# Performance work log

Measured on AMD Instinct MI355X. Metric: run time of the kernel, lower is better.

Reference implementation:

```python
import jax, jax.numpy as jnp
import numpy as np

N, E, D, L = 50000, 800000, 128, 2
NEG_SLOPE = 0.2
LN_EPS = 1e-5


def setup_inputs() -> dict:
    key = jax.random.key(0)
    ks = jax.random.split(key, 6)
    scale = 1.0 / np.sqrt(D)
    x = jax.random.normal(ks[0], (N, D), dtype=jnp.float32)
    edge_index = jax.random.randint(ks[1], (2, E), 0, N, dtype=jnp.int64)
    W = jax.random.normal(ks[2], (L, D, D), dtype=jnp.float32) * scale
    att_src = jax.random.normal(ks[3], (L, D), dtype=jnp.float32) * scale
    att_dst = jax.random.normal(ks[4], (L, D), dtype=jnp.float32) * scale
    bias = jnp.zeros((L, D), dtype=jnp.float32)
    gamma = jnp.ones((L, D), dtype=jnp.float32)
    beta = jnp.zeros((L, D), dtype=jnp.float32)
    return {"x": x, "edge_index": edge_index, "W": W, "att_src": att_src,
            "att_dst": att_dst, "bias": bias, "gamma": gamma, "beta": beta}


def reference(x, edge_index, W, att_src, att_dst, bias, gamma, beta):
    # PyG GATConv (heads=1, concat=True, add_self_loops=True), eval mode
    # (attention/feature dropout disabled), followed by residual + LayerNorm.
    n = x.shape[0]
    loops = jnp.arange(n, dtype=edge_index.dtype)
    ei = jnp.concatenate([edge_index, jnp.stack([loops, loops])], axis=1)
    src, dst = ei[0], ei[1]  # messages flow src -> dst
    for l in range(W.shape[0]):
        h = x @ W[l]                              # [N, D]
        a_src = h @ att_src[l]                    # [N]
        a_dst = h @ att_dst[l]                    # [N]
        logit = jax.nn.leaky_relu(a_src[src] + a_dst[dst], NEG_SLOPE)  # [E+N]
        # segment softmax over incoming edges of each dst node
        m = jax.ops.segment_max(logit, dst, num_segments=n)
        e = jnp.exp(logit - m[dst])
        s = jax.ops.segment_sum(e, dst, num_segments=n)
        alpha = e / s[dst]
        msg = h[src] * alpha[:, None]             # [E+N, D]
        x_att = jax.ops.segment_sum(msg, dst, num_segments=n) + bias[l]
        # residual + LayerNorm
        y = x + x_att
        mu = jnp.mean(y, axis=-1, keepdims=True)
        var = jnp.var(y, axis=-1, keepdims=True)
        x = (y - mu) * jax.lax.rsqrt(var + LN_EPS) * gamma[l] + beta[l]
    return x
```

## Files before the change

kernel.cpp:

```cpp
#include <hip/hip_runtime.h>
#include <hip/hip_fp16.h>

#define D 128
#define NSLOPE 0.2f
#define LN_EPS 1e-5f
#define CAP 6144

typedef unsigned int uint;
typedef float f32x4 __attribute__((ext_vector_type(4)));
typedef _Float16 f16x8 __attribute__((ext_vector_type(8)));

__device__ __forceinline__ float leaky(float x) { return x > 0.f ? x : NSLOPE * x; }
__device__ __forceinline__ uint pkh(float a, float b) {
    __half2 h = __floats2half2_rn(a, b);
    return *reinterpret_cast<uint*>(&h);
}
__device__ __forceinline__ float2 h2f(uint u) {
    __half2 h = *reinterpret_cast<__half2*>(&u);
    return __half22float2(h);
}
__device__ __forceinline__ __half2 u2h2(uint u) {
    return *reinterpret_cast<__half2*>(&u);
}

__global__ __launch_bounds__(256) void k_bucket(const int* __restrict__ ei,
        int* __restrict__ gcur, uint* __restrict__ staging, int e, int nbuck) {
    __shared__ uint pr[4096];
    __shared__ int hist[256], gbase[256], c2[256];
    int t = threadIdx.x;
    int base = blockIdx.x * 4096;
    hist[t] = 0;
    c2[t] = 0;
    int nv = min(4096, e - base);
    for (int j = t; j < nv; j += 256) {
        int i = base + j;
        pr[j] = ((uint)ei[e + i] << 16) | (uint)ei[i];
    }
    __syncthreads();
    for (int j = t; j < nv; j += 256)
        atomicAdd(&hist[pr[j] >> 24], 1);
    __syncthreads();
    if (t < nbuck && hist[t] > 0)
        gbase[t] = t * CAP + atomicAdd(&gcur[t], hist[t]);
    __syncthreads();
    for (int j = t; j < nv; j += 256) {
        uint p = pr[j];
        int b = p >> 24;
        int pos = atomicAdd(&c2[b], 1);
        staging[gbase[b] + pos] = p;
    }
}

__global__ __launch_bounds__(256) void k_bfill2(const uint* __restrict__ staging,
        const int* __restrict__ gcur, int* __restrict__ rowptr,
        int* __restrict__ csr, int n, int nb) {
    __shared__ int sb[256];
    __shared__ int h[256];
    __shared__ int lds[256];
    __shared__ int c2[256];
    int b = blockIdx.x, t = threadIdx.x;
    sb[t] = (t < nb) ? gcur[t] : 0;
    h[t] = 0;
    c2[t] = 0;
    __syncthreads();
    for (int off = 1; off < 256; off <<= 1) {
        int u = (t >= off) ? sb[t - off] : 0;
        __syncthreads();
        sb[t] += u;
        __syncthreads();
    }
    int ebase = (b == 0) ? 0 : sb[b - 1];
    int cnt = gcur[b];
    for (int i = t; i < cnt; i += 256)
        atomicAdd(&h[(staging[b * CAP + i] >> 16) & 255], 1);
    __syncthreads();
    int d = h[t];
    lds[t] = d;
    __syncthreads();
    for (int off = 1; off < 256; off <<= 1) {
        int u = (t >= off) ? lds[t - off] : 0;
        __syncthreads();
        lds[t] += u;
        __syncthreads();
    }
    int rp = ebase + lds[t] - d;
    int node = b * 256 + t;
    if (node < n) rowptr[node] = rp;
    if (b == 0 && t == 0) rowptr[n] = sb[nb - 1];
    __syncthreads();
    h[t] = rp;
    __syncthreads();
    for (int i = t; i < cnt; i += 256) {
        uint p = staging[b * CAP + i];
        int dn = (p >> 16) & 255;
        int r = atomicAdd(&c2[dn], 1);
        csr[h[dn] + r] = (int)(p & 0xffffu);
    }
}

__global__ __launch_bounds__(256) void k_wt(const float* __restrict__ W,
                                            uint* __restrict__ wth) {
    __shared__ float T[128][17];
    int t = threadIdx.x;
    int layer = blockIdx.x >> 3;
    int c0 = (blockIdx.x & 7) * 16;
    const float* Wl = W + (size_t)layer * D * D;
    uint* wl = wth + (size_t)layer * D * 64;
    #pragma unroll
    for (int pass = 0; pass < 2; ++pass) {
        int k = pass * 64 + (t >> 2);
        int c = (t & 3) * 4;
        float4 v = *(const float4*)&Wl[k * D + c0 + c];
        T[k][c] = v.x; T[k][c + 1] = v.y; T[k][c + 2] = v.z; T[k][c + 3] = v.w;
    }
    __syncthreads();
    int cw = t >> 4;
    int k0 = (t & 15) * 8;
    uint4 uh;
    uh.x = pkh(T[k0 + 0][cw], T[k0 + 1][cw]);
    uh.y = pkh(T[k0 + 2][cw], T[k0 + 3][cw]);
    uh.z = pkh(T[k0 + 4][cw], T[k0 + 5][cw]);
    uh.w = pkh(T[k0 + 6][cw], T[k0 + 7][cw]);
    *(uint4*)&wl[(c0 + cw) * 64 + (t & 15) * 4] = uh;
}

template <bool F16IN>
__global__ __launch_bounds__(256) void k_gemm2(const float* __restrict__ xf,
        const uint* __restrict__ xh, const uint* __restrict__ wth,
        const float* __restrict__ avs, const float* __restrict__ avd,
        uint* __restrict__ hb, float* __restrict__ asrc, float* __restrict__ adst, int n) {
    __shared__ char XH[64 * 256];
    __shared__ char WH[128 * 256];
    __shared__ float psL[256], pdL[256];

    int t = threadIdx.x;
    int brow = blockIdx.x * 64;
    int rows = min(64, n - brow);

    #pragma unroll
    for (int i = 0; i < 8; ++i) {
        int f = t + 256 * i;
        int row = f >> 5, k4 = f & 31;
        uint2 ph = make_uint2(0u, 0u);
        if (row < rows) {
            if (F16IN) {
                ph = *(const uint2*)&xh[(size_t)(brow + row) * 64 + k4 * 2];
            } else {
                float4 v = *(const float4*)&xf[(size_t)(brow + row) * D + k4 * 4];
                ph = make_uint2(pkh(v.x, v.y), pkh(v.z, v.w));
            }
        }
        int off = row * 256 + k4 * 8;
        int swz = (row & 7) << 4;
        *(uint2*)(XH + (off ^ swz)) = ph;
    }
    #pragma unroll
    for (int i = 0; i < 8; ++i) {
        int f = t + 256 * i;
        int col = f >> 4, j = f & 15;
        uint4 vh = *(const uint4*)&wth[col * 64 + j * 4];
        int off = col * 256 + j * 16;
        int swz = (col & 7) << 4;
        *(uint4*)(WH + (off ^ swz)) = vh;
    }
    __syncthreads();

    int wave = t >> 6, lane = t & 63;
    int l15 = lane & 15, lk = lane >> 4;

    f32x4 acc[4][2];
    #pragma unroll
    for (int rt = 0; rt < 4; ++rt)
        #pragma unroll
        for (int ct = 0; ct < 2; ++ct)
            acc[rt][ct] = (f32x4){0.f, 0.f, 0.f, 0.f};

    #pragma unroll
    for (int ks = 0; ks < 4; ++ks) {
        f16x8 a[4], b[2];
        #pragma unroll
        for (int rt = 0; rt < 4; ++rt) {
            int row = rt * 16 + l15;
            int off = row * 256 + (ks * 32 + lk * 8) * 2;
            int swz = (row & 7) << 4;
            a[rt] = *(const f16x8*)(XH + (off ^ swz));
        }
        #pragma unroll
        for (int ct = 0; ct < 2; ++ct) {
            int col = wave * 32 + ct * 16 + l15;
            int off = col * 256 + (ks * 32 + lk * 8) * 2;
            int swz = (col & 7) << 4;
            b[ct] = *(const f16x8*)(WH + (off ^ swz));
        }
        #pragma unroll
        for (int rt = 0; rt < 4; ++rt)
            #pragma unroll
            for (int ct = 0; ct < 2; ++ct)
                acc[rt][ct] = __builtin_amdgcn_mfma_f32_16x16x32_f16(a[rt], b[ct], acc[rt][ct], 0, 0, 0);
    }

    float avs_lo = avs[wave * 32 + l15], avs_hi = avs[wave * 32 + 16 + l15];
    float avd_lo = avd[wave * 32 + l15], avd_hi = avd[wave * 32 + 16 + l15];
    #pragma unroll
    for (int rt = 0; rt < 4; ++rt) {
        #pragma unroll
        for (int j = 0; j < 4; ++j) {
            float ps = acc[rt][0][j] * avs_lo + acc[rt][1][j] * avs_hi;
            float pd = acc[rt][0][j] * avd_lo + acc[rt][1][j] * avd_hi;
            #pragma unroll
            for (int off = 8; off; off >>= 1) {
                ps += __shfl_xor(ps, off);
                pd += __shfl_xor(pd, off);
            }
            int row = rt * 16 + lk * 4 + j;
            if (l15 == 0) { psL[wave * 64 + row] = ps; pdL[wave * 64 + row] = pd; }
        }
    }
    #pragma unroll
    for (int rt = 0; rt < 4; ++rt) {
        #pragma unroll
        for (int j = 0; j < 4; ++j) {
            int row = rt * 16 + lk * 4 + j;
            if (row < rows)
                hb[(size_t)(brow + row) * 64 + wave * 16 + l15] =
                    pkh(acc[rt][0][j], acc[rt][1][j]);
        }
    }
    __syncthreads();
    if (t < 64 && t < rows) {
        asrc[brow + t] = psL[t] + psL[64 + t] + psL[128 + t] + psL[192 + t];
        adst[brow + t] = pdL[t] + pdL[64 + t] + pdL[128 + t] + pdL[192 + t];
    }
}

template <int MODE>
__global__ __launch_bounds__(256) void k_attn(const float* __restrict__ xf,
        const uint* __restrict__ xh, const uint* __restrict__ hb,
        const float* __restrict__ asrc, const float* __restrict__ adst,
        const int* __restrict__ rowptr, const int* __restrict__ csr,
        const float* __restrict__ bias, const float* __restrict__ gamma,
        const float* __restrict__ beta, float* __restrict__ out,
        uint* __restrict__ outh, int n) {
    int node = blockIdx.x * 16 + (threadIdx.x >> 4);
    if (node >= n) return;
    int sl = threadIdx.x & 15;
    int base_lo = (sl >> 2) * 32 + (sl & 3) * 4;

    float a_i = adst[node];
    float slg = leaky(asrc[node] + a_i);
    int rs = rowptr[node], re = rowptr[node + 1];

    float m_g = slg, ssum = 1.f;
    __half2 acch[4];
    {
        uint4 q = *(const uint4*)&hb[(size_t)node * 64 + sl * 4];
        acch[0] = u2h2(q.x); acch[1] = u2h2(q.y);
        acch[2] = u2h2(q.z); acch[3] = u2h2(q.w);
    }

    for (int e = rs; e < re; e += 2) {
        int c1 = min(e + 1, re - 1);
        int s0 = csr[e], s1 = csr[c1];
        uint4 q0 = *(const uint4*)&hb[(size_t)s0 * 64 + sl * 4];
        uint4 q1 = *(const uint4*)&hb[(size_t)s1 * 64 + sl * 4];
        float lg0 = leaky(asrc[s0] + a_i);
        float lg1 = (e + 1 < re) ? leaky(asrc[s1] + a_i) : -1e30f;
        float nm = fmaxf(m_g, fmaxf(lg0, lg1));
        if (nm > m_g) {
            float sc = __expf(m_g - nm);
            ssum *= sc;
            __half2 sch = __half2half2(__float2half(sc));
            #pragma unroll
            for (int j = 0; j < 4; ++j) acch[j] = __hmul2(acch[j], sch);
            m_g = nm;
        }
        float w0 = __expf(lg0 - nm);
        float w1 = (e + 1 < re) ? __expf(lg1 - nm) : 0.f;
        ssum += w0 + w1;
        __half2 w0h = __half2half2(__float2half(w0));
        __half2 w1h = __half2half2(__float2half(w1));
        acch[0] = __hfma2(w0h, u2h2(q0.x), acch[0]);
        acch[1] = __hfma2(w0h, u2h2(q0.y), acch[1]);
        acch[2] = __hfma2(w0h, u2h2(q0.z), acch[2]);
        acch[3] = __hfma2(w0h, u2h2(q0.w), acch[3]);
        acch[0] = __hfma2(w1h, u2h2(q1.x), acch[0]);
        acch[1] = __hfma2(w1h, u2h2(q1.y), acch[1]);
        acch[2] = __hfma2(w1h, u2h2(q1.z), acch[2]);
        acch[3] = __hfma2(w1h, u2h2(q1.w), acch[3]);
    }

    float inv = 1.f / ssum;
    float acc[8];
    {
        float2 f0 = __half22float2(acch[0]);
        float2 f1 = __half22float2(acch[1]);
        float2 f2 = __half22float2(acch[2]);
        float2 f3 = __half22float2(acch[3]);
        acc[0] = f0.x * inv; acc[1] = f1.x * inv; acc[2] = f2.x * inv; acc[3] = f3.x * inv;
        acc[4] = f0.y * inv; acc[5] = f1.y * inv; acc[6] = f2.y * inv; acc[7] = f3.y * inv;
    }

    float x0, x1, x2, x3, x4, x5, x6, x7;
    if (MODE == 0) {
        float4 xa = *(const float4*)&xf[(size_t)node * D + base_lo];
        float4 xb = *(const float4*)&xf[(size_t)node * D + base_lo + 16];
        x0 = xa.x; x1 = xa.y; x2 = xa.z; x3 = xa.w;
        x4 = xb.x; x5 = xb.y; x6 = xb.z; x7 = xb.w;
    } else {
        uint2 ua = *(const uint2*)&xh[(size_t)node * 64 + (base_lo >> 1)];
        uint2 ub = *(const uint2*)&xh[(size_t)node * 64 + (base_lo >> 1) + 8];
        float2 fa0 = h2f(ua.x), fa1 = h2f(ua.y), fb0 = h2f(ub.x), fb1 = h2f(ub.y);
        x0 = fa0.x; x1 = fa0.y; x2 = fa1.x; x3 = fa1.y;
        x4 = fb0.x; x5 = fb0.y; x6 = fb1.x; x7 = fb1.y;
    }
    float4 ba = *(const float4*)&bias[base_lo];
    float4 bb = *(const float4*)&bias[base_lo + 16];
    float y[8];
    y[0] = x0 + acc[0] + ba.x;
    y[1] = x1 + acc[1] + ba.y;
    y[2] = x2 + acc[2] + ba.z;
    y[3] = x3 + acc[3] + ba.w;
    y[4] = x4 + acc[4] + bb.x;
    y[5] = x5 + acc[5] + bb.y;
    y[6] = x6 + acc[6] + bb.z;
    y[7] = x7 + acc[7] + bb.w;

    float s1 = 0.f, s2 = 0.f;
    #pragma unroll
    for (int j = 0; j < 8; ++j) { s1 += y[j]; s2 += y[j] * y[j]; }
    #pragma unroll
    for (int off = 1; off <= 8; off <<= 1) {
        s1 += __shfl_xor(s1, off);
        s2 += __shfl_xor(s2, off);
    }
    float mu = s1 * (1.f / D);
    float var = s2 * (1.f / D) - mu * mu;
    float rstd = rsqrtf(var + LN_EPS);

    float4 ga = *(const float4*)&gamma[base_lo];
    float4 gb = *(const float4*)&gamma[base_lo + 16];
    float4 bta = *(const float4*)&beta[base_lo];
    float4 btb = *(const float4*)&beta[base_lo + 16];
    float o0 = (y[0] - mu) * rstd * ga.x + bta.x;
    float o1 = (y[1] - mu) * rstd * ga.y + bta.y;
    float o2 = (y[2] - mu) * rstd * ga.z + bta.z;
    float o3 = (y[3] - mu) * rstd * ga.w + bta.w;
    float o4 = (y[4] - mu) * rstd * gb.x + btb.x;
    float o5 = (y[5] - mu) * rstd * gb.y + btb.y;
    float o6 = (y[6] - mu) * rstd * gb.z + btb.z;
    float o7 = (y[7] - mu) * rstd * gb.w + btb.w;
    if (MODE == 0) {
        uint2 oa = make_uint2(pkh(o0, o1), pkh(o2, o3));
        uint2 ob = make_uint2(pkh(o4, o5), pkh(o6, o7));
        *(uint2*)&outh[(size_t)node * 64 + (base_lo >> 1)] = oa;
        *(uint2*)&outh[(size_t)node * 64 + (base_lo >> 1) + 8] = ob;
    } else {
        *(float4*)&out[(size_t)node * D + base_lo] = make_float4(o0, o1, o2, o3);
        *(float4*)&out[(size_t)node * D + base_lo + 16] = make_float4(o4, o5, o6, o7);
    }
}

extern "C" void kernel_launch(void* const* d_in, const int* in_sizes, int n_in,
                              void* d_out, int out_size, void* d_ws, size_t ws_size,
                              hipStream_t stream) {
    const float* x       = (const float*)d_in[0];
    const int*   ei      = (const int*)d_in[1];
    const float* W       = (const float*)d_in[2];
    const float* att_src = (const float*)d_in[3];
    const float* att_dst = (const float*)d_in[4];
    const float* bias    = (const float*)d_in[5];
    const float* gamma   = (const float*)d_in[6];
    const float* beta    = (const float*)d_in[7];
    float* out = (float*)d_out;

    const int N = in_sizes[0] / D;
    const int E = in_sizes[1] / 2;
    const int NBUCK = (N + 255) / 256;

    char* base = (char*)d_ws;
    size_t off = 0;
    auto alloc = [&](size_t bytes) {
        char* p = base + off;
        off += (bytes + 255) & ~(size_t)255;
        return p;
    };
    uint*  hb      = (uint*)alloc((size_t)N * 64 * 4);
    uint*  xh16    = (uint*)alloc((size_t)N * 64 * 4);
    float* asrc    = (float*)alloc((size_t)N * 4);
    float* adst    = (float*)alloc((size_t)N * 4);
    int*   rowptr  = (int*)alloc((size_t)(N + 1) * 4);
    int*   csr     = (int*)alloc((size_t)E * 4);
    uint*  staging = (uint*)alloc((size_t)NBUCK * CAP * 4);
    int*   gcur    = (int*)alloc((size_t)NBUCK * 4);
    uint*  wth     = (uint*)alloc((size_t)2 * D * 64 * 4);

    hipMemsetAsync(gcur, 0, (size_t)NBUCK * 4, stream);
    k_bucket<<<(E + 4095) / 4096, 256, 0, stream>>>(ei, gcur, staging, E, NBUCK);
    k_bfill2<<<NBUCK, 256, 0, stream>>>(staging, gcur, rowptr, csr, N, NBUCK);
    k_wt<<<16, 256, 0, stream>>>(W, wth);

    const int nblk_node = (N + 15) / 16;
    const int nblk_gemm = (N + 63) / 64;

    k_gemm2<false><<<nblk_gemm, 256, 0, stream>>>(x, nullptr, wth, att_src, att_dst,
                                                  hb, asrc, adst, N);
    k_attn<0><<<nblk_node, 256, 0, stream>>>(x, nullptr, hb, asrc, adst, rowptr, csr,
                                             bias, gamma, beta, nullptr, xh16, N);
    k_gemm2<true><<<nblk_gemm, 256, 0, stream>>>(nullptr, xh16, wth + (size_t)D * 64,
                                                 att_src + D, att_dst + D,
                                                 hb, asrc, adst, N);
    k_attn<1><<<nblk_node, 256, 0, stream>>>(nullptr, xh16, hb, asrc, adst, rowptr, csr,
                                             bias + D, gamma + D, beta + D, out, nullptr, N);
}
```

Before: 145.8 us.

## Fuse edge bucketing into first GEMM launch and merge weight prep with counter reset

Folds the memset of the bucket counters into the weight-transpose kernel, and runs the edge-bucketing blocks in the same grid as the layer-0 GEMM blocks, selected by block index. This cuts launch count and lets the two independent stages overlap on the GPU instead of running one after the other. The fused kernel reserves the larger GEMM shared-memory footprint for every block, which may lower occupancy for the bucketing blocks.

New measurement: 137.9 us. 1.06x faster.

```diff
diff --git a/kernel.cpp b/kernel.cpp
--- a/kernel.cpp
+++ b/kernel.cpp
@@ -23,12 +23,45 @@
     return *reinterpret_cast<__half2*>(&u);
 }
 
-__global__ __launch_bounds__(256) void k_bucket(const int* __restrict__ ei,
-        int* __restrict__ gcur, uint* __restrict__ staging, int e, int nbuck) {
-    __shared__ uint pr[4096];
-    __shared__ int hist[256], gbase[256], c2[256];
+__global__ __launch_bounds__(256) void k_prep(const float* __restrict__ W,
+        uint* __restrict__ wth, int* __restrict__ gcur, int nbuck) {
+    __shared__ float T[128][17];
     int t = threadIdx.x;
-    int base = blockIdx.x * 4096;
+    if (blockIdx.x == 16) {
+        if (t < nbuck) gcur[t] = 0;
+        return;
+    }
+    int layer = blockIdx.x >> 3;
+    int c0 = (blockIdx.x & 7) * 16;
+    const float* Wl = W + (size_t)layer * D * D;
+    uint* wl = wth + (size_t)layer * D * 64;
+    #pragma unroll
+    for (int pass = 0; pass < 2; ++pass) {
+        int k = pass * 64 + (t >> 2);
+        int c = (t & 3) * 4;
+        float4 v = *(const float4*)&Wl[k * D + c0 + c];
+        T[k][c] = v.x; T[k][c + 1] = v.y; T[k][c + 2] = v.z; T[k][c + 3] = v.w;
+    }
+    __syncthreads();
+    int cw = t >> 4;
+    int k0 = (t & 15) * 8;
+    uint4 uh;
+    uh.x = pkh(T[k0 + 0][cw], T[k0 + 1][cw]);
+    uh.y = pkh(T[k0 + 2][cw], T[k0 + 3][cw]);
+    uh.z = pkh(T[k0 + 4][cw], T[k0 + 5][cw]);
+    uh.w = pkh(T[k0 + 6][cw], T[k0 + 7][cw]);
+    *(uint4*)&wl[(c0 + cw) * 64 + (t & 15) * 4] = uh;
+}
+
+__device__ __forceinline__ void bucket_body(char* SMEM, int bid,
+        const int* __restrict__ ei, int* __restrict__ gcur,
+        uint* __restrict__ staging, int e, int nbuck) {
+    uint* pr   = (uint*)SMEM;
+    int* hist  = (int*)(SMEM + 16384);
+    int* gbase = (int*)(SMEM + 17408);
+    int* c2    = (int*)(SMEM + 18432);
+    int t = threadIdx.x;
+    int base = bid * 4096;
     hist[t] = 0;
     c2[t] = 0;
     int nv = min(4096, e - base);
@@ -49,6 +82,138 @@
         int pos = atomicAdd(&c2[b], 1);
         staging[gbase[b] + pos] = p;
     }
+}
+
+template <bool F16IN>
+__device__ __forceinline__ void gemm_body(char* SMEM, int bid,
+        const float* __restrict__ xf, const uint* __restrict__ xh,
+        const uint* __restrict__ wth, const float* __restrict__ avs,
+        const float* __restrict__ avd, uint* __restrict__ hb,
+        float* __restrict__ asrc, float* __restrict__ adst, int n) {
+    char* XH   = SMEM;
+    char* WH   = SMEM + 16384;
+    float* psL = (float*)(SMEM + 49152);
+    float* pdL = (float*)(SMEM + 50176);
+
+    int t = threadIdx.x;
+    int brow = bid * 64;
+    int rows = min(64, n - brow);
+
+    #pragma unroll
+    for (int i = 0; i < 8; ++i) {
+        int f = t + 256 * i;
+        int row = f >> 5, k4 = f & 31;
+        uint2 ph = make_uint2(0u, 0u);
+        if (row < rows) {
+            if (F16IN) {
+                ph = *(const uint2*)&xh[(size_t)(brow + row) * 64 + k4 * 2];
+            } else {
+                float4 v = *(const float4*)&xf[(size_t)(brow + row) * D + k4 * 4];
+                ph = make_uint2(pkh(v.x, v.y), pkh(v.z, v.w));
+            }
+        }
+        int off = row * 256 + k4 * 8;
+        int swz = (row & 7) << 4;
+        *(uint2*)(XH + (off ^ swz)) = ph;
+    }
+    #pragma unroll
+    for (int i = 0; i < 8; ++i) {
+        int f = t + 256 * i;
+        int col = f >> 4, j = f & 15;
+        uint4 vh = *(const uint4*)&wth[col * 64 + j * 4];
+        int off = col * 256 + j * 16;
+        int swz = (col & 7) << 4;
+        *(uint4*)(WH + (off ^ swz)) = vh;
+    }
+    __syncthreads();
+
+    int wave = t >> 6, lane = t & 63;
+    int l15 = lane & 15, lk = lane >> 4;
+
+    f32x4 acc[4][2];
+    #pragma unroll
+    for (int rt = 0; rt < 4; ++rt)
+        #pragma unroll
+        for (int ct = 0; ct < 2; ++ct)
+            acc[rt][ct] = (f32x4){0.f, 0.f, 0.f, 0.f};
+
+    #pragma unroll
+    for (int ks = 0; ks < 4; ++ks) {
+        f16x8 a[4], b[2];
+        #pragma unroll
+        for (int rt = 0; rt < 4; ++rt) {
+            int row = rt * 16 + l15;
+            int off = row * 256 + (ks * 32 + lk * 8) * 2;
+            int swz = (row & 7) << 4;
+            a[rt] = *(const f16x8*)(XH + (off ^ swz));
+        }
+        #pragma unroll
+        for (int ct = 0; ct < 2; ++ct) {
+            int col = wave * 32 + ct * 16 + l15;
+            int off = col * 256 + (ks * 32 + lk * 8) * 2;
+            int swz = (col & 7) << 4;
+            b[ct] = *(const f16x8*)(WH + (off ^ swz));
+        }
+        #pragma unroll
+        for (int rt = 0; rt < 4; ++rt)
+            #pragma unroll
+            for (int ct = 0; ct < 2; ++ct)
+                acc[rt][ct] = __builtin_amdgcn_mfma_f32_16x16x32_f16(a[rt], b[ct], acc[rt][ct], 0, 0, 0);
+    }
+
+    float avs_lo = avs[wave * 32 + l15], avs_hi = avs[wave * 32 + 16 + l15];
+    float avd_lo = avd[wave * 32 + l15], avd_hi = avd[wave * 32 + 16 + l15];
+    #pragma unroll
+    for (int rt = 0; rt < 4; ++rt) {
+        #pragma unroll
+        for (int j = 0; j < 4; ++j) {
+            float ps = acc[rt][0][j] * avs_lo + acc[rt][1][j] * avs_hi;
+            float pd = acc[rt][0][j] * avd_lo + acc[rt][1][j] * avd_hi;
+            #pragma unroll
+            for (int off = 8; off; off >>= 1) {
+                ps += __shfl_xor(ps, off);
+                pd += __shfl_xor(pd, off);
+            }
+            int row = rt * 16 + lk * 4 + j;
+            if (l15 == 0) { psL[wave * 64 + row] = ps; pdL[wave * 64 + row] = pd; }
+        }
+    }
+    #pragma unroll
+    for (int rt = 0; rt < 4; ++rt) {
+        #pragma unroll
+        for (int j = 0; j < 4; ++j) {
+            int row = rt * 16 + lk * 4 + j;
+            if (row < rows)
+                hb[(size_t)(brow + row) * 64 + wave * 16 + l15] =
+                    pkh(acc[rt][0][j], acc[rt][1][j]);
+        }
+    }
+    __syncthreads();
+    if (t < 64 && t < rows) {
+        asrc[brow + t] = psL[t] + psL[64 + t] + psL[128 + t] + psL[192 + t];
+        adst[brow + t] = pdL[t] + pdL[64 + t] + pdL[128 + t] + pdL[192 + t];
+    }
+}
+
+__global__ __launch_bounds__(256) void k_fused0(const float* __restrict__ x,
+        const uint* __restrict__ wth, const float* __restrict__ avs,
+        const float* __restrict__ avd, uint* __restrict__ hb,
+        float* __restrict__ asrc, float* __restrict__ adst, int n,
+        const int* __restrict__ ei, int* __restrict__ gcur,
+        uint* __restrict__ staging, int e, int nbuck, int ngemm) {
+    __shared__ __align__(16) char SMEM[51200];
+    if ((int)blockIdx.x < ngemm)
+        gemm_body<false>(SMEM, blockIdx.x, x, nullptr, wth, avs, avd, hb, asrc, adst, n);
+    else
+        bucket_body(SMEM, blockIdx.x - ngemm, ei, gcur, staging, e, nbuck);
+}
+
+__global__ __launch_bounds__(256) void k_gemm_f16(const uint* __restrict__ xh,
+        const uint* __restrict__ wth, const float* __restrict__ avs,
+        const float* __restrict__ avd, uint* __restrict__ hb,
+        float* __restrict__ asrc, float* __restrict__ adst, int n) {
+    __shared__ __align__(16) char SMEM[51200];
+    gemm_body<true>(SMEM, blockIdx.x, nullptr, xh, wth, avs, avd, hb, asrc, adst, n);
 }
 
 __global__ __launch_bounds__(256) void k_bfill2(const uint* __restrict__ staging,
@@ -95,141 +260,6 @@
         int dn = (p >> 16) & 255;
         int r = atomicAdd(&c2[dn], 1);
         csr[h[dn] + r] = (int)(p & 0xffffu);
-    }
-}
-
-__global__ __launch_bounds__(256) void k_wt(const float* __restrict__ W,
-                                            uint* __restrict__ wth) {
-    __shared__ float T[128][17];
-    int t = threadIdx.x;
-    int layer = blockIdx.x >> 3;
-    int c0 = (blockIdx.x & 7) * 16;
-    const float* Wl = W + (size_t)layer * D * D;
-    uint* wl = wth + (size_t)layer * D * 64;
-    #pragma unroll
-    for (int pass = 0; pass < 2; ++pass) {
-        int k = pass * 64 + (t >> 2);
-        int c = (t & 3) * 4;
-        float4 v = *(const float4*)&Wl[k * D + c0 + c];
-        T[k][c] = v.x; T[k][c + 1] = v.y; T[k][c + 2] = v.z; T[k][c + 3] = v.w;
-    }
-    __syncthreads();
-    int cw = t >> 4;
-    int k0 = (t & 15) * 8;
-    uint4 uh;
-    uh.x = pkh(T[k0 + 0][cw], T[k0 + 1][cw]);
-    uh.y = pkh(T[k0 + 2][cw], T[k0 + 3][cw]);
-    uh.z = pkh(T[k0 + 4][cw], T[k0 + 5][cw]);
-    uh.w = pkh(T[k0 + 6][cw], T[k0 + 7][cw]);
-    *(uint4*)&wl[(c0 + cw) * 64 + (t & 15) * 4] = uh;
-}
-
-template <bool F16IN>
-__global__ __launch_bounds__(256) void k_gemm2(const float* __restrict__ xf,
-        const uint* __restrict__ xh, const uint* __restrict__ wth,
-        const float* __restrict__ avs, const float* __restrict__ avd,
-        uint* __restrict__ hb, float* __restrict__ asrc, float* __restrict__ adst, int n) {
-    __shared__ char XH[64 * 256];
-    __shared__ char WH[128 * 256];
-    __shared__ float psL[256], pdL[256];
-
-    int t = threadIdx.x;
-    int brow = blockIdx.x * 64;
-    int rows = min(64, n - brow);
-
-    #pragma unroll
-    for (int i = 0; i < 8; ++i) {
-        int f = t + 256 * i;
-        int row = f >> 5, k4 = f & 31;
-        uint2 ph = make_uint2(0u, 0u);
-        if (row < rows) {
-            if (F16IN) {
-                ph = *(const uint2*)&xh[(size_t)(brow + row) * 64 + k4 * 2];
-            } else {
-                float4 v = *(const float4*)&xf[(size_t)(brow + row) * D + k4 * 4];
-                ph = make_uint2(pkh(v.x, v.y), pkh(v.z, v.w));
-            }
-        }
-        int off = row * 256 + k4 * 8;
-        int swz = (row & 7) << 4;
-        *(uint2*)(XH + (off ^ swz)) = ph;
-    }
-    #pragma unroll
-    for (int i = 0; i < 8; ++i) {
-        int f = t + 256 * i;
-        int col = f >> 4, j = f & 15;
-        uint4 vh = *(const uint4*)&wth[col * 64 + j * 4];
-        int off = col * 256 + j * 16;
-        int swz = (col & 7) << 4;
-        *(uint4*)(WH + (off ^ swz)) = vh;
-    }
-    __syncthreads();
-
-    int wave = t >> 6, lane = t & 63;
-    int l15 = lane & 15, lk = lane >> 4;
-
-    f32x4 acc[4][2];
-    #pragma unroll
-    for (int rt = 0; rt < 4; ++rt)
-        #pragma unroll
-        for (int ct = 0; ct < 2; ++ct)
-            acc[rt][ct] = (f32x4){0.f, 0.f, 0.f, 0.f};
-
-    #pragma unroll
-    for (int ks = 0; ks < 4; ++ks) {
-        f16x8 a[4], b[2];
-        #pragma unroll
-        for (int rt = 0; rt < 4; ++rt) {
-            int row = rt * 16 + l15;
-            int off = row * 256 + (ks * 32 + lk * 8) * 2;
-            int swz = (row & 7) << 4;
-            a[rt] = *(const f16x8*)(XH + (off ^ swz));
-        }
-        #pragma unroll
-        for (int ct = 0; ct < 2; ++ct) {
-            int col = wave * 32 + ct * 16 + l15;
-            int off = col * 256 + (ks * 32 + lk * 8) * 2;
-            int swz = (col & 7) << 4;
-            b[ct] = *(const f16x8*)(WH + (off ^ swz));
-        }
-        #pragma unroll
-        for (int rt = 0; rt < 4; ++rt)
-            #pragma unroll
-            for (int ct = 0; ct < 2; ++ct)
-                acc[rt][ct] = __builtin_amdgcn_mfma_f32_16x16x32_f16(a[rt], b[ct], acc[rt][ct], 0, 0, 0);
-    }
-
-    float avs_lo = avs[wave * 32 + l15], avs_hi = avs[wave * 32 + 16 + l15];
-    float avd_lo = avd[wave * 32 + l15], avd_hi = avd[wave * 32 + 16 + l15];
-    #pragma unroll
-    for (int rt = 0; rt < 4; ++rt) {
-        #pragma unroll
-        for (int j = 0; j < 4; ++j) {
-            float ps = acc[rt][0][j] * avs_lo + acc[rt][1][j] * avs_hi;
-            float pd = acc[rt][0][j] * avd_lo + acc[rt][1][j] * avd_hi;
-            #pragma unroll
-            for (int off = 8; off; off >>= 1) {
-                ps += __shfl_xor(ps, off);
-                pd += __shfl_xor(pd, off);
-            }
-            int row = rt * 16 + lk * 4 + j;
-            if (l15 == 0) { psL[wave * 64 + row] = ps; pdL[wave * 64 + row] = pd; }
-        }
-    }
-    #pragma unroll
-    for (int rt = 0; rt < 4; ++rt) {
-        #pragma unroll
-        for (int j = 0; j < 4; ++j) {
-            int row = rt * 16 + lk * 4 + j;
-            if (row < rows)
-                hb[(size_t)(brow + row) * 64 + wave * 16 + l15] =
-                    pkh(acc[rt][0][j], acc[rt][1][j]);
-        }
-    }
-    __syncthreads();
-    if (t < 64 && t < rows) {
-        asrc[brow + t] = psL[t] + psL[64 + t] + psL[128 + t] + psL[192 + t];
-        adst[brow + t] = pdL[t] + pdL[64 + t] + pdL[128 + t] + pdL[192 + t];
     }
 }
 
@@ -394,21 +424,20 @@
     int*   gcur    = (int*)alloc((size_t)NBUCK * 4);
     uint*  wth     = (uint*)alloc((size_t)2 * D * 64 * 4);
 
-    hipMemsetAsync(gcur, 0, (size_t)NBUCK * 4, stream);
-    k_bucket<<<(E + 4095) / 4096, 256, 0, stream>>>(ei, gcur, staging, E, NBUCK);
-    k_bfill2<<<NBUCK, 256, 0, stream>>>(staging, gcur, rowptr, csr, N, NBUCK);
-    k_wt<<<16, 256, 0, stream>>>(W, wth);
-
     const int nblk_node = (N + 15) / 16;
     const int nblk_gemm = (N + 63) / 64;
-
-    k_gemm2<false><<<nblk_gemm, 256, 0, stream>>>(x, nullptr, wth, att_src, att_dst,
-                                                  hb, asrc, adst, N);
+    const int nblk_buck = (E + 4095) / 4096;
+
+    k_prep<<<17, 256, 0, stream>>>(W, wth, gcur, NBUCK);
+    k_fused0<<<nblk_gemm + nblk_buck, 256, 0, stream>>>(
+        x, wth, att_src, att_dst, hb, asrc, adst, N,
+        ei, gcur, staging, E, NBUCK, nblk_gemm);
+    k_bfill2<<<NBUCK, 256, 0, stream>>>(staging, gcur, rowptr, csr, N, NBUCK);
     k_attn<0><<<nblk_node, 256, 0, stream>>>(x, nullptr, hb, asrc, adst, rowptr, csr,
                                              bias, gamma, beta, nullptr, xh16, N);
-    k_gemm2<true><<<nblk_gemm, 256, 0, stream>>>(nullptr, xh16, wth + (size_t)D * 64,
-                                                 att_src + D, att_dst + D,
-                                                 hb, asrc, adst, N);
+    k_gemm_f16<<<nblk_gemm, 256, 0, stream>>>(xh16, wth + (size_t)D * 64,
+                                              att_src + D, att_dst + D,
+                                              hb, asrc, adst, N);
     k_attn<1><<<nblk_node, 256, 0, stream>>>(nullptr, xh16, hb, asrc, adst, rowptr, csr,
                                              bias + D, gamma + D, beta + D, out, nullptr, N);
 }
```
